# Kernel tuning notes

Hardware: AMD Instinct MI355X
Metric: run time of the kernel (lower is better)

## Reference

```python
import jax, jax.numpy as jnp
import numpy as np

H, L, NB = 128, 2048, 64  # features, seq len, half state size (conj-symmetric N=128)


def _forward(u, x_re, x_im, Lambda_re, Lambda_im, B_re, B_im, C_re, C_im, D, d):
    Lam = (Lambda_re + 1j * Lambda_im).astype(jnp.complex64)   # (H, NB) discrete diag A
    B = (B_re + 1j * B_im).astype(jnp.complex64)               # (H, NB)
    C = (C_re + 1j * C_im).astype(jnp.complex64)               # (H, NB)
    x0 = (x_re + 1j * x_im).astype(jnp.complex64)              # (H, NB) initial state
    Hn, Ln = u.shape
    # scan elements (A_t, b_t, d_t); identity element (1, x0, False) prepended at t=0
    A = jnp.concatenate([jnp.ones((Hn, 1, NB), jnp.complex64),
                         jnp.broadcast_to(Lam[:, None, :], (Hn, Ln, NB))], axis=1)
    b = jnp.concatenate([x0[:, None, :],
                         B[:, None, :] * u[:, :, None].astype(jnp.complex64)], axis=1)
    dd = jnp.concatenate([jnp.zeros((1,), bool), d.astype(bool)])[None, :, None]  # (1, L+1, 1)

    def combine(lhs, rhs):
        # reset-aware associative combine: if right done-flag set, drop left contribution
        A_i, b_i, c_i = lhs
        A_j, b_j, c_j = rhs
        return (jnp.where(c_j, A_j, A_j * A_i),
                jnp.where(c_j, b_j, A_j * b_i + b_j),
                jnp.logical_or(c_i, c_j))

    _, xs, _ = jax.lax.associative_scan(combine, (A, b, dd), axis=1)
    xs = xs[:, 1:]                                             # (H, L, NB) hidden states
    # conj symmetry: y_t = 2*Re(C @ x_t) + D * u_t
    y = 2.0 * jnp.real(jnp.einsum('hn,hln->hl', C, xs)) + D[:, None] * u
    return y, xs[:, -1]


def setup_inputs():
    key = jax.random.key(0)
    ks = jax.random.split(key, 8)
    # stable ZOH-discretized HiPPO-like diagonal system (mirrors LSSL-f init)
    dts = jnp.logspace(-3.0, -1.0, H)                          # (H,) per-feature timescales
    k = jnp.arange(NB, dtype=jnp.float32)
    lam_c = -0.5 + 1j * jnp.pi * (2.0 * k + 1.0)               # (NB,) continuous poles
    lam_d = jnp.exp(dts[:, None] * lam_c[None, :]).astype(jnp.complex64)  # (H, NB), |.|<1
    Bc = ((jax.random.normal(ks[0], (NB,)) + 1j * jax.random.normal(ks[1], (NB,)))
          / jnp.sqrt(2.0 * NB)).astype(jnp.complex64)
    Bd = (((lam_d - 1.0) / lam_c[None, :]) * Bc[None, :]).astype(jnp.complex64)  # (H, NB)
    C = ((jax.random.normal(ks[2], (H, NB)) + 1j * jax.random.normal(ks[3], (H, NB)))
         / jnp.sqrt(float(NB))).astype(jnp.complex64)
    return {
        "u": jax.random.normal(ks[4], (H, L), jnp.float32),
        "x_re": jnp.zeros((H, NB), jnp.float32),
        "x_im": jnp.zeros((H, NB), jnp.float32),
        "Lambda_re": jnp.real(lam_d).astype(jnp.float32),
        "Lambda_im": jnp.imag(lam_d).astype(jnp.float32),
        "B_re": jnp.real(Bd).astype(jnp.float32),
        "B_im": jnp.imag(Bd).astype(jnp.float32),
        "C_re": jnp.real(C).astype(jnp.float32),
        "C_im": jnp.imag(C).astype(jnp.float32),
        "D": jax.random.normal(ks[5], (H,), jnp.float32),
        "d": jax.random.bernoulli(ks[6], 0.01, (L,)),
    }


def reference(u, x_re, x_im, Lambda_re, Lambda_im, B_re, B_im, C_re, C_im, D, d):
    return _forward(u, x_re, x_im, Lambda_re, Lambda_im, B_re, B_im, C_re, C_im, D, d)
```

## Files before the change

### kernel.cpp

```cpp
#include <hip/hip_runtime.h>

#define Hn 128
#define Ln 2048
#define NBn 64
#define K 64
#define G 32
#define PITCH 65


__global__ __launch_bounds__(64) void phase1_local(
    const float* __restrict__ u,
    const float* __restrict__ Lre,  const float* __restrict__ Lim,
    const float* __restrict__ Bre,  const float* __restrict__ Bim,
    const float* __restrict__ Cre,  const float* __restrict__ Cim,
    const float* __restrict__ Dv,   const int* __restrict__ dflag,
    float* __restrict__ out,
    float4* __restrict__ Sum)
{
    __shared__ float g_s[K * PITCH];
    __shared__ float u_s[K];

    const int g = blockIdx.x, h = blockIdx.y, n = threadIdx.x;
    const int hn = h * NBn + n;
    const int l0 = g * K;

    const float lre = Lre[hn], lim = Lim[hn];
    const float br  = Bre[hn], bi  = Bim[hn];
    const float cr  = Cre[hn], ci  = Cim[hn];
    const float Dh  = Dv[h];
    const float cbr2 = 2.f * (cr * br - ci * bi);
    const float cbi2 = 2.f * (cr * bi + ci * br);

    u_s[n] = u[h * Ln + l0 + n];
    const unsigned long long m = __ballot(dflag[l0 + n] != 0);
    __syncthreads();

    float wr = 0.f, wi = 0.f;
    if (m == 0ull) {
        #pragma unroll
        for (int k = 0; k < K; ++k) {
            const float uk = u_s[k];
            const float nr = fmaf(lre, wr, fmaf(-lim, wi, cbr2 * uk));
            const float ni = fmaf(lre, wi, fmaf( lim, wr, cbi2 * uk));
            wr = nr; wi = ni;
            g_s[k * PITCH + n] = wr;
        }
    } else {
        #pragma unroll
        for (int k = 0; k < K; ++k) {
            const bool  rs  = (m >> k) & 1ull;
            const float lrk = rs ? 0.f : lre;
            const float lik = rs ? 0.f : lim;
            const float uk  = u_s[k];
            const float nr = fmaf(lrk, wr, fmaf(-lik, wi, cbr2 * uk));
            const float ni = fmaf(lrk, wi, fmaf( lik, wr, cbi2 * uk));
            wr = nr; wi = ni;
            g_s[k * PITCH + n] = wr;
        }
    }
    __syncthreads();

    const float* row = g_s + n * PITCH;
    float a0 = 0.f, a1 = 0.f, a2 = 0.f, a3 = 0.f;
    #pragma unroll
    for (int k = 0; k < NBn; k += 4) {
        a0 += row[k + 0]; a1 += row[k + 1];
        a2 += row[k + 2]; a3 += row[k + 3];
    }
    out[h * Ln + l0 + n] = (a0 + a1) + (a2 + a3) + Dh * u_s[n];

    float pr = lre, pi = lim;
    #pragma unroll
    for (int it = 0; it < 6; ++it) {
        const float sr2 = pr * pr - pi * pi;
        const float si2 = 2.f * pr * pi;
        pr = sr2; pi = si2;
    }
    if (m) { pr = 0.f; pi = 0.f; }
    Sum[(h * G + g) * NBn + n] = make_float4(pr, pi, wr, wi);
}

__global__ __launch_bounds__(64) void phase2_combine(
    const float* __restrict__ x_re, const float* __restrict__ x_im,
    const float* __restrict__ Cre,  const float* __restrict__ Cim,
    const float4* __restrict__ Sum,
    float2* __restrict__ Sin,
    float* __restrict__ out)
{
    const int h = blockIdx.x, n = threadIdx.x;
    const int hn = h * NBn + n;
    const float cr = Cre[hn], ci = Cim[hn];
    const float x0r = x_re[hn], x0i = x_im[hn];
    float sre = 2.f * (cr * x0r - ci * x0i);
    float sim = 2.f * (cr * x0i + ci * x0r);
    #pragma unroll
    for (int g = 0; g < G; ++g) {
        const int idx = (h * G + g) * NBn + n;
        const float4 s = Sum[idx];
        Sin[idx] = make_float2(sre, sim);
        const float nr = fmaf(s.x, sre, fmaf(-s.y, sim, s.z));
        const float ni = fmaf(s.x, sim, fmaf( s.y, sre, s.w));
        sre = nr; sim = ni;
    }
    const float c2r = 2.f * cr, c2i = 2.f * ci;
    const float inv = 1.f / (c2r * c2r + c2i * c2i);
    float* xlast = out + Hn * Ln;
    xlast[2 * hn + 0] = (sre * c2r + sim * c2i) * inv;
    xlast[2 * hn + 1] = (sim * c2r - sre * c2i) * inv;
}

__global__ __launch_bounds__(64) void phase3_fixup(
    const float* __restrict__ Lre, const float* __restrict__ Lim,
    const int* __restrict__ dflag,
    const float2* __restrict__ Sin,
    float* __restrict__ out)
{
    __shared__ float g_s[K * PITCH];

    const int g = blockIdx.x, h = blockIdx.y, n = threadIdx.x;
    const int hn = h * NBn + n;
    const int l0 = g * K;

    const float2 s = Sin[(h * G + g) * NBn + n];
    const float lre = Lre[hn], lim = Lim[hn];

    const unsigned long long bal = __ballot(dflag[l0 + n] != 0);
    const int kr = bal ? (__ffsll((long long)bal) - 1) : K;

    const float l2r = lre * lre - lim * lim;
    const float l2i = 2.f * lre * lim;

    float tAr = fmaf(lre, s.x, -lim * s.y);
    float tAi = fmaf(lre, s.y,  lim * s.x);
    float tBr = fmaf(l2r, s.x, -l2i * s.y);
    float tBi = fmaf(l2r, s.y,  l2i * s.x);
    g_s[0 * PITCH + n] = tAr;
    g_s[1 * PITCH + n] = tBr;
    #pragma unroll
    for (int k = 2; k < K; k += 2) {
        const float nAr = fmaf(l2r, tAr, -l2i * tAi);
        const float nAi = fmaf(l2r, tAi,  l2i * tAr);
        tAr = nAr; tAi = nAi;
        g_s[k * PITCH + n] = tAr;
        const float nBr = fmaf(l2r, tBr, -l2i * tBi);
        const float nBi = fmaf(l2r, tBi,  l2i * tBr);
        tBr = nBr; tBi = nBi;
        g_s[(k + 1) * PITCH + n] = tBr;
    }
    __syncthreads();

    const float* row = g_s + n * PITCH;
    float a0 = 0.f, a1 = 0.f, a2 = 0.f, a3 = 0.f;
    #pragma unroll
    for (int k = 0; k < NBn; k += 4) {
        a0 += row[k + 0]; a1 += row[k + 1];
        a2 += row[k + 2]; a3 += row[k + 3];
    }
    if (n < kr)
        out[h * Ln + l0 + n] += (a0 + a1) + (a2 + a3);
}

extern "C" void kernel_launch(void* const* d_in, const int* in_sizes, int n_in,
                              void* d_out, int out_size, void* d_ws, size_t ws_size,
                              hipStream_t stream) {
    const float* u    = (const float*)d_in[0];
    const float* x_re = (const float*)d_in[1];
    const float* x_im = (const float*)d_in[2];
    const float* Lre  = (const float*)d_in[3];
    const float* Lim  = (const float*)d_in[4];
    const float* Bre  = (const float*)d_in[5];
    const float* Bim  = (const float*)d_in[6];
    const float* Cre  = (const float*)d_in[7];
    const float* Cim  = (const float*)d_in[8];
    const float* Dv   = (const float*)d_in[9];
    const int*   dfl  = (const int*)d_in[10];
    float* out = (float*)d_out;

    const int HGN = Hn * G * NBn;
    float4* Sum = (float4*)d_ws;
    float2* Sin = (float2*)(Sum + HGN);

    dim3 grid(G, Hn);
    phase1_local<<<grid, 64, 0, stream>>>(u, Lre, Lim, Bre, Bim, Cre, Cim,
                                          Dv, dfl, out, Sum);
    phase2_combine<<<Hn, 64, 0, stream>>>(x_re, x_im, Cre, Cim, Sum, Sin, out);
    phase3_fixup<<<grid, 64, 0, stream>>>(Lre, Lim, dfl, Sin, out);
}
```

Measured before the change: 88.65 us.

## Fuse chunk-carry combine into fixup kernel by recomputing prefix per block

Removes the separate serial combine kernel by having each fixup block recompute the carry-in state, walking the chunk summaries of all preceding chunks itself. This saves one kernel launch and the round trip of the Sin intermediate through global memory. In exchange, each block redundantly reads up to 32 float4 summaries and does O(G) serial complex FMAs, so total work becomes quadratic in chunk count. The last block also writes the final state.

```diff
diff --git a/kernel.cpp b/kernel.cpp
--- a/kernel.cpp
+++ b/kernel.cpp
@@ -80,39 +80,12 @@
     Sum[(h * G + g) * NBn + n] = make_float4(pr, pi, wr, wi);
 }
 
-__global__ __launch_bounds__(64) void phase2_combine(
+__global__ __launch_bounds__(64) void phase23_fixup(
     const float* __restrict__ x_re, const float* __restrict__ x_im,
+    const float* __restrict__ Lre,  const float* __restrict__ Lim,
     const float* __restrict__ Cre,  const float* __restrict__ Cim,
+    const int* __restrict__ dflag,
     const float4* __restrict__ Sum,
-    float2* __restrict__ Sin,
-    float* __restrict__ out)
-{
-    const int h = blockIdx.x, n = threadIdx.x;
-    const int hn = h * NBn + n;
-    const float cr = Cre[hn], ci = Cim[hn];
-    const float x0r = x_re[hn], x0i = x_im[hn];
-    float sre = 2.f * (cr * x0r - ci * x0i);
-    float sim = 2.f * (cr * x0i + ci * x0r);
-    #pragma unroll
-    for (int g = 0; g < G; ++g) {
-        const int idx = (h * G + g) * NBn + n;
-        const float4 s = Sum[idx];
-        Sin[idx] = make_float2(sre, sim);
-        const float nr = fmaf(s.x, sre, fmaf(-s.y, sim, s.z));
-        const float ni = fmaf(s.x, sim, fmaf( s.y, sre, s.w));
-        sre = nr; sim = ni;
-    }
-    const float c2r = 2.f * cr, c2i = 2.f * ci;
-    const float inv = 1.f / (c2r * c2r + c2i * c2i);
-    float* xlast = out + Hn * Ln;
-    xlast[2 * hn + 0] = (sre * c2r + sim * c2i) * inv;
-    xlast[2 * hn + 1] = (sim * c2r - sre * c2i) * inv;
-}
-
-__global__ __launch_bounds__(64) void phase3_fixup(
-    const float* __restrict__ Lre, const float* __restrict__ Lim,
-    const int* __restrict__ dflag,
-    const float2* __restrict__ Sin,
     float* __restrict__ out)
 {
     __shared__ float g_s[K * PITCH];
@@ -121,19 +94,44 @@
     const int hn = h * NBn + n;
     const int l0 = g * K;
 
-    const float2 s = Sin[(h * G + g) * NBn + n];
+    const float cr = Cre[hn], ci = Cim[hn];
+    const float x0r = x_re[hn], x0i = x_im[hn];
+    float sre = 2.f * (cr * x0r - ci * x0i);
+    float sim = 2.f * (cr * x0i + ci * x0r);
+
+    const float4* base = Sum + h * G * NBn + n;
+    #pragma unroll
+    for (int j = 0; j < G; ++j) {
+        const float4 s = base[j * NBn];
+        if (j < g) {
+            const float nr = fmaf(s.x, sre, fmaf(-s.y, sim, s.z));
+            const float ni = fmaf(s.x, sim, fmaf( s.y, sre, s.w));
+            sre = nr; sim = ni;
+        }
+    }
+
+    if (g == G - 1) {
+        const float4 s = base[(G - 1) * NBn];
+        const float fr = fmaf(s.x, sre, fmaf(-s.y, sim, s.z));
+        const float fi = fmaf(s.x, sim, fmaf( s.y, sre, s.w));
+        const float c2r = 2.f * cr, c2i = 2.f * ci;
+        const float inv = 1.f / (c2r * c2r + c2i * c2i);
+        float* xlast = out + Hn * Ln;
+        xlast[2 * hn + 0] = (fr * c2r + fi * c2i) * inv;
+        xlast[2 * hn + 1] = (fi * c2r - fr * c2i) * inv;
+    }
+
     const float lre = Lre[hn], lim = Lim[hn];
-
     const unsigned long long bal = __ballot(dflag[l0 + n] != 0);
     const int kr = bal ? (__ffsll((long long)bal) - 1) : K;
 
     const float l2r = lre * lre - lim * lim;
     const float l2i = 2.f * lre * lim;
 
-    float tAr = fmaf(lre, s.x, -lim * s.y);
-    float tAi = fmaf(lre, s.y,  lim * s.x);
-    float tBr = fmaf(l2r, s.x, -l2i * s.y);
-    float tBi = fmaf(l2r, s.y,  l2i * s.x);
+    float tAr = fmaf(lre, sre, -lim * sim);
+    float tAi = fmaf(lre, sim,  lim * sre);
+    float tBr = fmaf(l2r, sre, -l2i * sim);
+    float tBi = fmaf(l2r, sim,  l2i * sre);
     g_s[0 * PITCH + n] = tAr;
     g_s[1 * PITCH + n] = tBr;
     #pragma unroll
@@ -176,13 +174,11 @@
     const int*   dfl  = (const int*)d_in[10];
     float* out = (float*)d_out;
 
-    const int HGN = Hn * G * NBn;
     float4* Sum = (float4*)d_ws;
-    float2* Sin = (float2*)(Sum + HGN);
 
     dim3 grid(G, Hn);
     phase1_local<<<grid, 64, 0, stream>>>(u, Lre, Lim, Bre, Bim, Cre, Cim,
                                           Dv, dfl, out, Sum);
-    phase2_combine<<<Hn, 64, 0, stream>>>(x_re, x_im, Cre, Cim, Sum, Sin, out);
-    phase3_fixup<<<grid, 64, 0, stream>>>(Lre, Lim, dfl, Sin, out);
+    phase23_fixup<<<grid, 64, 0, stream>>>(x_re, x_im, Lre, Lim, Cre, Cim,
+                                           dfl, Sum, out);
 }
```

Measured after the change: 107.2 us. +20.9%, slower.

## Switch from scan-then-fixup to summary-then-rescan chunked scan scheme

Applied to the files above, without the earlier changes.

Phase 1 now only computes each chunk's end-state summary and no longer writes outputs or per-step states to shared memory. Phase 3 then reruns the chunk recurrence seeded with the carried-in state from the combine pass and writes the final outputs directly. This replaces the separate fixup pass (power propagation plus a read-modify-write of the output) with a single output write. The price is running the recurrence twice, with u, B and C loaded again in the third kernel.

```diff
diff --git a/kernel.cpp b/kernel.cpp
--- a/kernel.cpp
+++ b/kernel.cpp
@@ -8,14 +8,100 @@
 #define PITCH 65
 
 
-__global__ __launch_bounds__(64) void phase1_local(
+__global__ __launch_bounds__(64) void k1_summary(
+    const float* __restrict__ u,
+    const float* __restrict__ Lre,  const float* __restrict__ Lim,
+    const float* __restrict__ Bre,  const float* __restrict__ Bim,
+    const float* __restrict__ Cre,  const float* __restrict__ Cim,
+    const int* __restrict__ dflag,
+    float4* __restrict__ Sum)
+{
+    __shared__ float u_s[K];
+
+    const int g = blockIdx.x, h = blockIdx.y, n = threadIdx.x;
+    const int hn = h * NBn + n;
+    const int l0 = g * K;
+
+    const float lre = Lre[hn], lim = Lim[hn];
+    const float br  = Bre[hn], bi  = Bim[hn];
+    const float cr  = Cre[hn], ci  = Cim[hn];
+    const float cbr2 = 2.f * (cr * br - ci * bi);
+    const float cbi2 = 2.f * (cr * bi + ci * br);
+
+    u_s[n] = u[h * Ln + l0 + n];
+    const unsigned long long m = __ballot(dflag[l0 + n] != 0);
+    __syncthreads();
+
+    float wr = 0.f, wi = 0.f;
+    if (m == 0ull) {
+        #pragma unroll
+        for (int k = 0; k < K; ++k) {
+            const float uk = u_s[k];
+            const float nr = fmaf(lre, wr, fmaf(-lim, wi, cbr2 * uk));
+            const float ni = fmaf(lre, wi, fmaf( lim, wr, cbi2 * uk));
+            wr = nr; wi = ni;
+        }
+    } else {
+        #pragma unroll
+        for (int k = 0; k < K; ++k) {
+            const bool  rs  = (m >> k) & 1ull;
+            const float lrk = rs ? 0.f : lre;
+            const float lik = rs ? 0.f : lim;
+            const float uk  = u_s[k];
+            const float nr = fmaf(lrk, wr, fmaf(-lik, wi, cbr2 * uk));
+            const float ni = fmaf(lrk, wi, fmaf( lik, wr, cbi2 * uk));
+            wr = nr; wi = ni;
+        }
+    }
+
+    float pr = lre, pi = lim;
+    #pragma unroll
+    for (int it = 0; it < 6; ++it) {
+        const float sr2 = pr * pr - pi * pi;
+        const float si2 = 2.f * pr * pi;
+        pr = sr2; pi = si2;
+    }
+    if (m) { pr = 0.f; pi = 0.f; }
+    Sum[(h * G + g) * NBn + n] = make_float4(pr, pi, wr, wi);
+}
+
+__global__ __launch_bounds__(64) void k2_combine(
+    const float* __restrict__ x_re, const float* __restrict__ x_im,
+    const float* __restrict__ Cre,  const float* __restrict__ Cim,
+    const float4* __restrict__ Sum,
+    float2* __restrict__ Sin,
+    float* __restrict__ out)
+{
+    const int h = blockIdx.x, n = threadIdx.x;
+    const int hn = h * NBn + n;
+    const float cr = Cre[hn], ci = Cim[hn];
+    const float x0r = x_re[hn], x0i = x_im[hn];
+    float sre = 2.f * (cr * x0r - ci * x0i);
+    float sim = 2.f * (cr * x0i + ci * x0r);
+    #pragma unroll
+    for (int g = 0; g < G; ++g) {
+        const int idx = (h * G + g) * NBn + n;
+        const float4 s = Sum[idx];
+        Sin[idx] = make_float2(sre, sim);
+        const float nr = fmaf(s.x, sre, fmaf(-s.y, sim, s.z));
+        const float ni = fmaf(s.x, sim, fmaf( s.y, sre, s.w));
+        sre = nr; sim = ni;
+    }
+    const float c2r = 2.f * cr, c2i = 2.f * ci;
+    const float inv = 1.f / (c2r * c2r + c2i * c2i);
+    float* xlast = out + Hn * Ln;
+    xlast[2 * hn + 0] = (sre * c2r + sim * c2i) * inv;
+    xlast[2 * hn + 1] = (sim * c2r - sre * c2i) * inv;
+}
+
+__global__ __launch_bounds__(64) void k3_rescan(
     const float* __restrict__ u,
     const float* __restrict__ Lre,  const float* __restrict__ Lim,
     const float* __restrict__ Bre,  const float* __restrict__ Bim,
     const float* __restrict__ Cre,  const float* __restrict__ Cim,
     const float* __restrict__ Dv,   const int* __restrict__ dflag,
-    float* __restrict__ out,
-    float4* __restrict__ Sum)
+    const float2* __restrict__ Sin,
+    float* __restrict__ out)
 {
     __shared__ float g_s[K * PITCH];
     __shared__ float u_s[K];
@@ -31,11 +117,13 @@
     const float cbr2 = 2.f * (cr * br - ci * bi);
     const float cbi2 = 2.f * (cr * bi + ci * br);
 
-    u_s[n] = u[h * Ln + l0 + n];
+    const float2 win = Sin[(h * G + g) * NBn + n];
+    const float ul = u[h * Ln + l0 + n];
+    u_s[n] = ul;
     const unsigned long long m = __ballot(dflag[l0 + n] != 0);
     __syncthreads();
 
-    float wr = 0.f, wi = 0.f;
+    float wr = win.x, wi = win.y;
     if (m == 0ull) {
         #pragma unroll
         for (int k = 0; k < K; ++k) {
@@ -67,97 +155,7 @@
         a0 += row[k + 0]; a1 += row[k + 1];
         a2 += row[k + 2]; a3 += row[k + 3];
     }
-    out[h * Ln + l0 + n] = (a0 + a1) + (a2 + a3) + Dh * u_s[n];
-
-    float pr = lre, pi = lim;
-    #pragma unroll
-    for (int it = 0; it < 6; ++it) {
-        const float sr2 = pr * pr - pi * pi;
-        const float si2 = 2.f * pr * pi;
-        pr = sr2; pi = si2;
-    }
-    if (m) { pr = 0.f; pi = 0.f; }
-    Sum[(h * G + g) * NBn + n] = make_float4(pr, pi, wr, wi);
-}
-
-__global__ __launch_bounds__(64) void phase2_combine(
-    const float* __restrict__ x_re, const float* __restrict__ x_im,
-    const float* __restrict__ Cre,  const float* __restrict__ Cim,
-    const float4* __restrict__ Sum,
-    float2* __restrict__ Sin,
-    float* __restrict__ out)
-{
-    const int h = blockIdx.x, n = threadIdx.x;
-    const int hn = h * NBn + n;
-    const float cr = Cre[hn], ci = Cim[hn];
-    const float x0r = x_re[hn], x0i = x_im[hn];
-    float sre = 2.f * (cr * x0r - ci * x0i);
-    float sim = 2.f * (cr * x0i + ci * x0r);
-    #pragma unroll
-    for (int g = 0; g < G; ++g) {
-        const int idx = (h * G + g) * NBn + n;
-        const float4 s = Sum[idx];
-        Sin[idx] = make_float2(sre, sim);
-        const float nr = fmaf(s.x, sre, fmaf(-s.y, sim, s.z));
-        const float ni = fmaf(s.x, sim, fmaf( s.y, sre, s.w));
-        sre = nr; sim = ni;
-    }
-    const float c2r = 2.f * cr, c2i = 2.f * ci;
-    const float inv = 1.f / (c2r * c2r + c2i * c2i);
-    float* xlast = out + Hn * Ln;
-    xlast[2 * hn + 0] = (sre * c2r + sim * c2i) * inv;
-    xlast[2 * hn + 1] = (sim * c2r - sre * c2i) * inv;
-}
-
-__global__ __launch_bounds__(64) void phase3_fixup(
-    const float* __restrict__ Lre, const float* __restrict__ Lim,
-    const int* __restrict__ dflag,
-    const float2* __restrict__ Sin,
-    float* __restrict__ out)
-{
-    __shared__ float g_s[K * PITCH];
-
-    const int g = blockIdx.x, h = blockIdx.y, n = threadIdx.x;
-    const int hn = h * NBn + n;
-    const int l0 = g * K;
-
-    const float2 s = Sin[(h * G + g) * NBn + n];
-    const float lre = Lre[hn], lim = Lim[hn];
-
-    const unsigned long long bal = __ballot(dflag[l0 + n] != 0);
-    const int kr = bal ? (__ffsll((long long)bal) - 1) : K;
-
-    const float l2r = lre * lre - lim * lim;
-    const float l2i = 2.f * lre * lim;
-
-    float tAr = fmaf(lre, s.x, -lim * s.y);
-    float tAi = fmaf(lre, s.y,  lim * s.x);
-    float tBr = fmaf(l2r, s.x, -l2i * s.y);
-    float tBi = fmaf(l2r, s.y,  l2i * s.x);
-    g_s[0 * PITCH + n] = tAr;
-    g_s[1 * PITCH + n] = tBr;
-    #pragma unroll
-    for (int k = 2; k < K; k += 2) {
-        const float nAr = fmaf(l2r, tAr, -l2i * tAi);
-        const float nAi = fmaf(l2r, tAi,  l2i * tAr);
-        tAr = nAr; tAi = nAi;
-        g_s[k * PITCH + n] = tAr;
-        const float nBr = fmaf(l2r, tBr, -l2i * tBi);
-        const float nBi = fmaf(l2r, tBi,  l2i * tBr);
-        tBr = nBr; tBi = nBi;
-        g_s[(k + 1) * PITCH + n] = tBr;
-    }
-    __syncthreads();
-
-    const float* row = g_s + n * PITCH;
-    float a0 = 0.f, a1 = 0.f, a2 = 0.f, a3 = 0.f;
-    #pragma unroll
-    for (int k = 0; k < NBn; k += 4) {
-        a0 += row[k + 0]; a1 += row[k + 1];
-        a2 += row[k + 2]; a3 += row[k + 3];
-    }
-    if (n < kr)
-        out[h * Ln + l0 + n] += (a0 + a1) + (a2 + a3);
+    out[h * Ln + l0 + n] = (a0 + a1) + (a2 + a3) + Dh * ul;
 }
 
 extern "C" void kernel_launch(void* const* d_in, const int* in_sizes, int n_in,
@@ -181,8 +179,9 @@
     float2* Sin = (float2*)(Sum + HGN);
 
     dim3 grid(G, Hn);
-    phase1_local<<<grid, 64, 0, stream>>>(u, Lre, Lim, Bre, Bim, Cre, Cim,
-                                          Dv, dfl, out, Sum);
-    phase2_combine<<<Hn, 64, 0, stream>>>(x_re, x_im, Cre, Cim, Sum, Sin, out);
-    phase3_fixup<<<grid, 64, 0, stream>>>(Lre, Lim, dfl, Sin, out);
+    k1_summary<<<grid, 64, 0, stream>>>(u, Lre, Lim, Bre, Bim, Cre, Cim,
+                                        dfl, Sum);
+    k2_combine<<<Hn, 64, 0, stream>>>(x_re, x_im, Cre, Cim, Sum, Sin, out);
+    k3_rescan<<<grid, 64, 0, stream>>>(u, Lre, Lim, Bre, Bim, Cre, Cim,
+                                       Dv, dfl, Sin, out);
 }
```

Result: no change. 89.07 us (+0.5%).
